# Performance work log

Hardware: AMD Instinct MI355X
Metric: run time of the kernel (lower is better)

## Reference

```python
import jax, jax.numpy as jnp
import numpy as np

NUM_HEADS = 8
OUT_FEATURES = 64
ALPHA = 0.2


def setup_inputs() -> dict:
    key = jax.random.key(0)
    k1, k2, k3, k4 = jax.random.split(key, 4)
    B, N, E, F_IN = 2, 8192, 4096, 256
    x = jax.random.normal(k1, (B, N, F_IN), dtype=jnp.float32)
    H = jax.random.uniform(k2, (N, E), dtype=jnp.float32)
    # xavier-like scaled params
    W = jax.random.normal(k3, (F_IN, OUT_FEATURES * NUM_HEADS), dtype=jnp.float32) * 0.05
    a_vertices = jax.random.normal(k4, (OUT_FEATURES, 1), dtype=jnp.float32) * 0.1
    return {"x": x, "H": H, "W": W, "a_vertices": a_vertices}


def reference(x, H, W, a_vertices):
    B, N, _ = x.shape
    # Wh: (B, N, heads, out)
    Wh = jnp.matmul(x, W).reshape(B, N, NUM_HEADS, OUT_FEATURES)
    # per-node, per-head attention logit: (B, N, heads)
    av = jax.nn.leaky_relu(jnp.einsum('bnhd,d->bnh', Wh, a_vertices[:, 0]), ALPHA)
    # edge attention: softmax over edges (torch dim=0 of (E, heads))
    ae = jax.nn.softmax(jnp.einsum('ne,bnh->beh', H, av), axis=1)  # (B, E, heads)
    # aggregate node features onto edges: (B, E, heads, out)
    m = jnp.einsum('ne,bnhd->behd', H, Wh)
    # scatter back to nodes with edge-attention weighting: (B, N, heads, out)
    out = jnp.einsum('ne,beh,behd->bnhd', H, ae, m)
    return out.reshape(B, N, NUM_HEADS * OUT_FEATURES)
```

## Files before the change

kernel.cpp:

```cpp
#include <hip/hip_runtime.h>

#define N_NODES 8192
#define N_EDGES 4096
#define F_INS   256
#define HEADS   8
#define DOUT    64
#define HDIM    512
#define CCOMB   1024
#define BATCH   2

typedef __bf16 bf16x8 __attribute__((ext_vector_type(8)));
typedef __bf16 bf16x4 __attribute__((ext_vector_type(4)));
typedef float  f32x4  __attribute__((ext_vector_type(4)));

__device__ __forceinline__ void gld_lds16(const __bf16* g, __bf16* l) {
    __builtin_amdgcn_global_load_lds(
        (const __attribute__((address_space(1))) void*)g,
        (__attribute__((address_space(3))) void*)l, 16, 0, 0);
}

__launch_bounds__(256)
__global__ void convert_H_logits_kernel(const float* __restrict__ H,
                                        const float* __restrict__ av,
                                        __bf16* __restrict__ Hb,
                                        __bf16* __restrict__ HbT,
                                        float* __restrict__ logits) {
    __shared__ float lav[512 * 16];
    __shared__ __bf16 tile[32][33];
    __shared__ float red[256 * 16];
    int t = threadIdx.x;
    int e0 = blockIdx.x * 32;
    int n0 = blockIdx.y * 512;
    for (int p = t; p < 8192; p += 256) {
        int b = p >> 12, rem = p & 4095, i = rem >> 3, h = rem & 7;
        lav[i * 16 + b * 8 + h] = av[(size_t)b * (N_NODES * 8) + (size_t)(n0 + i) * 8 + h];
    }
    __syncthreads();
    int c = t & 31, r0 = t >> 5;
    float acc[16];
#pragma unroll
    for (int q = 0; q < 16; ++q) acc[q] = 0.f;
    for (int sub = 0; sub < 16; ++sub) {
        int nb = n0 + sub * 32;
#pragma unroll
        for (int p = 0; p < 4; ++p) {
            int r = p * 8 + r0;
            float v = H[(size_t)(nb + r) * N_EDGES + e0 + c];
            __bf16 bv = (__bf16)v;
            Hb[(size_t)(nb + r) * N_EDGES + e0 + c] = bv;
            tile[r][c] = bv;
            const float* lr = &lav[(sub * 32 + r) * 16];
#pragma unroll
            for (int q = 0; q < 16; ++q) acc[q] += v * lr[q];
        }
        __syncthreads();
#pragma unroll
        for (int p = 0; p < 4; ++p) {
            int er = p * 8 + r0;
            HbT[(size_t)(e0 + er) * N_NODES + nb + c] = tile[c][er];
        }
        __syncthreads();
    }
#pragma unroll
    for (int q = 0; q < 16; ++q) red[t * 16 + q] = acc[q];
    __syncthreads();
    for (int o = t; o < 512; o += 256) {
        int e = o & 31, q = o >> 5;
        float s = 0.f;
#pragma unroll
        for (int r8 = 0; r8 < 8; ++r8) s += red[(r8 * 32 + e) * 16 + q];
        atomicAdd(&logits[(size_t)q * N_EDGES + e0 + e], s);
    }
}

__launch_bounds__(256)
__global__ void wbt_kernel(const float* __restrict__ W, __bf16* __restrict__ WbT) {
    int i = blockIdx.x * 256 + threadIdx.x;
    int c = i >> 8, f = i & 255;
    WbT[i] = (__bf16)W[(size_t)f * HDIM + c];
}

__launch_bounds__(256)
__global__ void wa_kernel(const float* __restrict__ W, const float* __restrict__ a,
                          float* __restrict__ Wa) {
    int i = blockIdx.x * 256 + threadIdx.x;
    if (i >= F_INS * HEADS) return;
    int f = i >> 3, h = i & 7;
    float s = 0.f;
#pragma unroll 8
    for (int d = 0; d < DOUT; ++d) s += W[(size_t)f * HDIM + h * DOUT + d] * a[d];
    Wa[i] = s;
}

__launch_bounds__(256)
__global__ void av_kernel(const float* __restrict__ x, const float* __restrict__ Wa,
                          float* __restrict__ av, __bf16* __restrict__ xb) {
    __shared__ float lx[32][257];
    __shared__ float lwa[F_INS * HEADS];
    int t = threadIdx.x;
    size_t row0 = (size_t)blockIdx.x * 32;
    for (int p = t; p < F_INS * HEADS; p += 256) lwa[p] = Wa[p];
#pragma unroll
    for (int p = 0; p < 32; ++p) {
        float v = x[(row0 + p) * F_INS + t];
        lx[p][t] = v;
        xb[(row0 + p) * F_INS + t] = (__bf16)v;
    }
    __syncthreads();
    int r = t >> 3, h = t & 7;
    float acc = 0.f;
#pragma unroll 8
    for (int f = 0; f < F_INS; ++f) acc += lx[r][f] * lwa[f * 8 + h];
    av[(row0 + r) * 8 + h] = acc > 0.f ? acc : 0.2f * acc;
}

__launch_bounds__(256)
__global__ void softmax_kernel(float* __restrict__ logits) {
    __shared__ float red[4];
    __shared__ float reds[4];
    int t = threadIdx.x;
    float* row = logits + (size_t)blockIdx.x * N_EDGES;
    float mx = -1e30f;
    for (int i = t; i < N_EDGES; i += 256) mx = fmaxf(mx, row[i]);
#pragma unroll
    for (int o = 32; o > 0; o >>= 1) mx = fmaxf(mx, __shfl_xor(mx, o, 64));
    if ((t & 63) == 0) red[t >> 6] = mx;
    __syncthreads();
    mx = fmaxf(fmaxf(red[0], red[1]), fmaxf(red[2], red[3]));
    float s = 0.f;
    for (int i = t; i < N_EDGES; i += 256) {
        float v = expf(row[i] - mx);
        row[i] = v;
        s += v;
    }
#pragma unroll
    for (int o = 32; o > 0; o >>= 1) s += __shfl_xor(s, o, 64);
    if ((t & 63) == 0) reds[t >> 6] = s;
    __syncthreads();
    float inv = 1.0f / (reds[0] + reds[1] + reds[2] + reds[3]);
    for (int i = t; i < N_EDGES; i += 256) row[i] *= inv;
}

template <int MODE>
__launch_bounds__(256, 4)
__global__ void gemm_bt(const __bf16* __restrict__ A, const __bf16* __restrict__ BT,
                        int lda, int ldbt, int K,
                        size_t a_bz, size_t bt_bz, size_t out_z,
                        __bf16* __restrict__ outB, int ldo,
                        float* __restrict__ outF) {
    __shared__ __bf16 AsF[8192];
    __shared__ __bf16 BsF[8192];
    int t = threadIdx.x;
    int bz = blockIdx.z;
    A  += (size_t)bz * a_bz;
    BT += (size_t)bz * bt_bz;
    if (MODE == 0) outB += (size_t)bz * out_z;
    if (MODE == 1) outF += (size_t)bz * out_z;
    size_t m0 = (size_t)blockIdx.y * 128;
    size_t n0 = (size_t)blockIdx.x * 128;

    int lane = t & 63, wv = t >> 6;
    int ln = lane & 15, lk = lane >> 4;

    const __bf16* pA[4]; const __bf16* pB[4];
    __bf16* lA[4]; __bf16* lB[4];
#pragma unroll
    for (int p = 0; p < 4; ++p) {
        int bid = wv * 4 + p;
        int mb = bid >> 1, kb = bid & 1;
        pA[p] = A + (m0 + mb * 16 + ln) * (size_t)lda + kb * 32 + lk * 8;
        pB[p] = BT + (n0 + mb * 16 + ln) * (size_t)ldbt + kb * 32 + lk * 8;
        lA[p] = &AsF[bid * 512];
        lB[p] = &BsF[bid * 512];
    }

    int wm16 = (wv & 1) * 4, wn16 = (wv >> 1) * 4;
    f32x4 acc[4][4] = {};

    for (int k0 = 0; k0 < K; k0 += 64) {
        __syncthreads();
#pragma unroll
        for (int p = 0; p < 4; ++p) gld_lds16(pA[p] + k0, lA[p]);
#pragma unroll
        for (int p = 0; p < 4; ++p) gld_lds16(pB[p] + k0, lB[p]);
        __syncthreads();
#pragma unroll
        for (int ksb = 0; ksb < 2; ++ksb) {
            bf16x8 af[4], bfr[4];
#pragma unroll
            for (int i = 0; i < 4; ++i)
                af[i] = *(const bf16x8*)&AsF[((wm16 + i) * 2 + ksb) * 512 + lane * 8];
#pragma unroll
            for (int j = 0; j < 4; ++j)
                bfr[j] = *(const bf16x8*)&BsF[((wn16 + j) * 2 + ksb) * 512 + lane * 8];
#pragma unroll
            for (int i = 0; i < 4; ++i)
#pragma unroll
                for (int j = 0; j < 4; ++j)
                    acc[i][j] = __builtin_amdgcn_mfma_f32_16x16x32_bf16(
                        af[i], bfr[j], acc[i][j], 0, 0, 0);
        }
    }

    int wm = (wv & 1) * 64, wn = (wv >> 1) * 64;
#pragma unroll
    for (int i = 0; i < 4; ++i)
#pragma unroll
        for (int j = 0; j < 4; ++j)
#pragma unroll
            for (int rg = 0; rg < 4; ++rg) {
                int gm = (int)m0 + wm + i * 16 + lk * 4 + rg;
                int gc = (int)n0 + wn + j * 16 + ln;
                float v = acc[i][j][rg];
                if (MODE == 0) {
                    outB[(size_t)gm * ldo + gc] = (__bf16)v;
                } else if (MODE == 1) {
                    outF[(size_t)gm * ldo + gc] = v;
                } else {
                    outF[(size_t)(gc >> 9) * ((size_t)N_NODES * HDIM) +
                         (size_t)gm * HDIM + (gc & 511)] = v;
                }
            }
}

__launch_bounds__(256)
__global__ void scale1_kernel(const float* __restrict__ acc1, const float* __restrict__ ae,
                              __bf16* __restrict__ mwT) {
    int i = blockIdx.x * 256 + threadIdx.x;
    size_t base = (size_t)i * 4;
    int c = (int)(base >> 12);
    int e = (int)(base & 4095);
    const size_t slab = (size_t)CCOMB * N_EDGES / 4;
    float4 s0 = ((const float4*)acc1)[i];
    float4 s1 = ((const float4*)acc1)[i + slab];
    float4 s2 = ((const float4*)acc1)[i + 2 * slab];
    float4 s3 = ((const float4*)acc1)[i + 3 * slab];
    float4 a4 = *(const float4*)(ae + ((size_t)(c >> 6) << 12) + e);
    bf16x4 o;
    o.x = (__bf16)((s0.x + s1.x + s2.x + s3.x) * a4.x);
    o.y = (__bf16)((s0.y + s1.y + s2.y + s3.y) * a4.y);
    o.z = (__bf16)((s0.z + s1.z + s2.z + s3.z) * a4.z);
    o.w = (__bf16)((s0.w + s1.w + s2.w + s3.w) * a4.w);
    ((bf16x4*)mwT)[i] = o;
}

extern "C" void kernel_launch(void* const* d_in, const int* in_sizes, int n_in,
                              void* d_out, int out_size, void* d_ws, size_t ws_size,
                              hipStream_t stream) {
    const float* x = (const float*)d_in[0];
    const float* H = (const float*)d_in[1];
    const float* W = (const float*)d_in[2];
    const float* a = (const float*)d_in[3];
    float* out = (float*)d_out;

    char* p = (char*)d_ws;
    __bf16* Hb   = (__bf16*)p; p += (size_t)N_NODES * N_EDGES * 2;
    __bf16* HbT  = (__bf16*)p; p += (size_t)N_EDGES * N_NODES * 2;
    __bf16* xb   = (__bf16*)p; p += (size_t)BATCH * N_NODES * F_INS * 2;
    __bf16* WbT  = (__bf16*)p; p += (size_t)HDIM * F_INS * 2;
    __bf16* WhbT = (__bf16*)p; p += (size_t)CCOMB * N_NODES * 2;
    __bf16* mwT  = (__bf16*)p; p += (size_t)CCOMB * N_EDGES * 2;
    float*  Wa   = (float*)p;  p += (size_t)F_INS * HEADS * 4;
    float*  av   = (float*)p;  p += (size_t)BATCH * N_NODES * HEADS * 4;
    float*  ae   = (float*)p;  p += (size_t)16 * N_EDGES * 4;
    float*  acc1 = (float*)p;  p += (size_t)4 * CCOMB * N_EDGES * 4;

    hipMemsetAsync(ae, 0, (size_t)16 * N_EDGES * 4, stream);

    wbt_kernel<<<dim3(HDIM * F_INS / 256), 256, 0, stream>>>(W, WbT);
    wa_kernel<<<dim3(8), 256, 0, stream>>>(W, a, Wa);
    av_kernel<<<dim3(BATCH * N_NODES / 32), 256, 0, stream>>>(x, Wa, av, xb);
    convert_H_logits_kernel<<<dim3(N_EDGES / 32, N_NODES / 512), 256, 0, stream>>>(
        H, av, Hb, HbT, ae);
    softmax_kernel<<<dim3(16), 256, 0, stream>>>(ae);

    gemm_bt<0><<<dim3(64, 4, 2), 256, 0, stream>>>(
        WbT, xb, F_INS, F_INS, F_INS,
        0, (size_t)N_NODES * F_INS, (size_t)HDIM * N_NODES,
        WhbT, N_NODES, nullptr);

    gemm_bt<1><<<dim3(32, 8, 4), 256, 0, stream>>>(
        WhbT, HbT, N_NODES, N_NODES, 2048,
        2048, 2048, (size_t)CCOMB * N_EDGES,
        nullptr, N_EDGES, acc1);

    scale1_kernel<<<dim3(CCOMB * N_EDGES / 4 / 256), 256, 0, stream>>>(acc1, ae, mwT);

    gemm_bt<2><<<dim3(8, 64, 1), 256, 0, stream>>>(
        Hb, mwT, N_EDGES, N_EDGES, N_EDGES,
        0, 0, 0,
        nullptr, 0, out);
}
```

Measured before the change: 567.2 us.

## Remap GEMM block indices for XCD-aware L2 locality and batch LDS fragment loads

Flattens the grids of the two large GEMMs to 1D and remaps block IDs so that blocks landing on the same XCD share A/B tiles, aiming for better L2 reuse across the chiplets. All LDS fragment loads for both k-subblocks are issued before the MFMA chain so that LDS latency overlaps better. The launch-bounds occupancy hint is lowered from 4 to 3 to leave room for the extra fragment registers, which may reduce waves per CU.

```diff
diff --git a/kernel.cpp b/kernel.cpp
--- a/kernel.cpp
+++ b/kernel.cpp
@@ -142,7 +142,7 @@
 }
 
 template <int MODE>
-__launch_bounds__(256, 4)
+__launch_bounds__(256, 3)
 __global__ void gemm_bt(const __bf16* __restrict__ A, const __bf16* __restrict__ BT,
                         int lda, int ldbt, int K,
                         size_t a_bz, size_t bt_bz, size_t out_z,
@@ -151,13 +151,28 @@
     __shared__ __bf16 AsF[8192];
     __shared__ __bf16 BsF[8192];
     int t = threadIdx.x;
-    int bz = blockIdx.z;
+
+    int bx, by, bz;
+    if (MODE == 0) {
+        bx = blockIdx.x; by = blockIdx.y; bz = blockIdx.z;
+    } else if (MODE == 1) {
+        int bid = blockIdx.x;
+        int xcd = bid & 7, local = bid >> 3;
+        bz = local >> 5;
+        int rem = local & 31;
+        bx = xcd * 4 + (rem >> 3);
+        by = rem & 7;
+    } else {
+        int bid = blockIdx.x;
+        bx = bid & 7; by = bid >> 3; bz = 0;
+    }
+
     A  += (size_t)bz * a_bz;
     BT += (size_t)bz * bt_bz;
     if (MODE == 0) outB += (size_t)bz * out_z;
     if (MODE == 1) outF += (size_t)bz * out_z;
-    size_t m0 = (size_t)blockIdx.y * 128;
-    size_t n0 = (size_t)blockIdx.x * 128;
+    size_t m0 = (size_t)by * 128;
+    size_t n0 = (size_t)bx * 128;
 
     int lane = t & 63, wv = t >> 6;
     int ln = lane & 15, lk = lane >> 4;
@@ -184,22 +199,24 @@
 #pragma unroll
         for (int p = 0; p < 4; ++p) gld_lds16(pB[p] + k0, lB[p]);
         __syncthreads();
+        bf16x8 af[2][4], bfr[2][4];
 #pragma unroll
         for (int ksb = 0; ksb < 2; ++ksb) {
-            bf16x8 af[4], bfr[4];
 #pragma unroll
             for (int i = 0; i < 4; ++i)
-                af[i] = *(const bf16x8*)&AsF[((wm16 + i) * 2 + ksb) * 512 + lane * 8];
+                af[ksb][i] = *(const bf16x8*)&AsF[((wm16 + i) * 2 + ksb) * 512 + lane * 8];
 #pragma unroll
             for (int j = 0; j < 4; ++j)
-                bfr[j] = *(const bf16x8*)&BsF[((wn16 + j) * 2 + ksb) * 512 + lane * 8];
+                bfr[ksb][j] = *(const bf16x8*)&BsF[((wn16 + j) * 2 + ksb) * 512 + lane * 8];
+        }
+#pragma unroll
+        for (int ksb = 0; ksb < 2; ++ksb)
 #pragma unroll
             for (int i = 0; i < 4; ++i)
 #pragma unroll
                 for (int j = 0; j < 4; ++j)
                     acc[i][j] = __builtin_amdgcn_mfma_f32_16x16x32_bf16(
-                        af[i], bfr[j], acc[i][j], 0, 0, 0);
-        }
+                        af[ksb][i], bfr[ksb][j], acc[i][j], 0, 0, 0);
     }
 
     int wm = (wv & 1) * 64, wn = (wv >> 1) * 64;
@@ -279,14 +296,14 @@
         0, (size_t)N_NODES * F_INS, (size_t)HDIM * N_NODES,
         WhbT, N_NODES, nullptr);
 
-    gemm_bt<1><<<dim3(32, 8, 4), 256, 0, stream>>>(
+    gemm_bt<1><<<dim3(1024), 256, 0, stream>>>(
         WhbT, HbT, N_NODES, N_NODES, 2048,
         2048, 2048, (size_t)CCOMB * N_EDGES,
         nullptr, N_EDGES, acc1);
 
     scale1_kernel<<<dim3(CCOMB * N_EDGES / 4 / 256), 256, 0, stream>>>(acc1, ae, mwT);
 
-    gemm_bt<2><<<dim3(8, 64, 1), 256, 0, stream>>>(
+    gemm_bt<2><<<dim3(512), 256, 0, stream>>>(
         Hb, mwT, N_EDGES, N_EDGES, N_EDGES,
         0, 0, 0,
         nullptr, 0, out);
```

Result: no change. 568.0 us (+0.1%).
